# Optimization experiments

Hardware: AMD Instinct MI355X
Metric: run time of the kernel (lower is better)

Reference implementation:

```python
import jax, jax.numpy as jnp
import numpy as np

SCALING = 2.0  # alpha / r = 128 / 64


def setup_inputs() -> dict:
    key = jax.random.key(0)
    k1, k2, k3, k4 = jax.random.split(key, 4)
    in_f, out_f, r, tokens = 4096, 16384, 64, 64
    return {
        "x": jax.random.normal(k1, (tokens, in_f), dtype=jnp.float32),
        "weight": jax.random.normal(k2, (out_f, in_f), dtype=jnp.float32) * (1.0 / np.sqrt(in_f)),
        "lora_A": jax.random.normal(k3, (r, in_f), dtype=jnp.float32) * (1.0 / np.sqrt(in_f)),
        "lora_B": jax.random.normal(k4, (out_f, r), dtype=jnp.float32) * (1.0 / np.sqrt(r)),
    }


def reference(x, weight, lora_A, lora_B):
    # base GEMM: [T, in] @ [in, out] -> [T, out]
    base = x @ weight.T
    # low-rank adapter: ((x @ A^T) @ B^T) scaled
    lora = (x @ lora_A.T) @ lora_B.T
    return base + SCALING * lora
```

## Files before the change

kernel.cpp:

```cpp
#include <hip/hip_runtime.h>
#include <hip/hip_bf16.h>

typedef __attribute__((ext_vector_type(8))) short bf16x8;
typedef __attribute__((ext_vector_type(4))) short s16x4;
typedef __attribute__((ext_vector_type(4))) float f32x4;

__device__ __forceinline__ short f2b(float f) {
    __hip_bfloat16 h = __float2bfloat16(f);
    return __builtin_bit_cast(short, h);
}

#define NPH 16
#define KC  256

__global__ void prep_kernel(const float* __restrict__ x,
                            const float* __restrict__ A,
                            ushort* __restrict__ xb,
                            ushort* __restrict__ yb) {
    const int tid = threadIdx.x, bid = blockIdx.x;

    const int gid = bid * 256 + tid;
    if (gid < 65536) {
        float4 v = ((const float4*)x)[gid];
        ushort4 s;
        s.x = (ushort)f2b(v.x); s.y = (ushort)f2b(v.y);
        s.z = (ushort)f2b(v.z); s.w = (ushort)f2b(v.w);
        ((ushort4*)xb)[gid] = s;
    }

    const int wave = tid >> 6, lane = tid & 63;
    const int idx = bid * 4 + wave;
    const int t = idx >> 6, r = idx & 63;
    const float4* xr = (const float4*)(x + (size_t)t * 4096);
    const float4* ar = (const float4*)(A + (size_t)r * 4096);
    float s = 0.f;
    #pragma unroll
    for (int i = 0; i < 16; ++i) {
        float4 a = xr[i * 64 + lane];
        float4 b = ar[i * 64 + lane];
        s += a.x * b.x + a.y * b.y + a.z * b.z + a.w * b.w;
    }
    #pragma unroll
    for (int off = 32; off; off >>= 1) s += __shfl_xor(s, off, 64);
    if (lane == 0) yb[idx] = (ushort)f2b(2.0f * s);
}

__global__ void __launch_bounds__(512)
lora_gemm(const float* __restrict__ W,
          const float* __restrict__ Bm,
          const ushort* __restrict__ xb,
          const ushort* __restrict__ yb,
          float* __restrict__ out) {
    __shared__ ushort buf[2][64 * KC];

    const int tid  = threadIdx.x;
    const int w    = tid >> 6;
    const int lane = tid & 63;
    const int j0   = blockIdx.x << 6;

    if (w >= 4) {
        const int s = w - 4;
        f32x4 st[16];
        for (int p = 0; p < NPH; ++p) {
            char* dst = (char*)&buf[p & 1][0];
            #pragma unroll
            for (int i = 0; i < 16; ++i) {
                const float* src = W + (size_t)(j0 + s * 16 + i) * 4096
                                     + p * KC + lane * 4;
                st[i] = *(const f32x4*)src;
            }
            #pragma unroll
            for (int i = 0; i < 16; ++i) {
                const int q = s * 16 + i;
                s16x4 v;
                v[0] = f2b(st[i][0]); v[1] = f2b(st[i][1]);
                v[2] = f2b(st[i][2]); v[3] = f2b(st[i][3]);
                *(s16x4*)(dst + q * 512 + ((lane * 8) ^ ((q & 7) << 4))) = v;
            }
            asm volatile("s_waitcnt lgkmcnt(0)" ::: "memory");
            __builtin_amdgcn_s_barrier();
        }
        return;
    }

    const int c  = lane & 15;
    const int kg = lane >> 4;
    const ushort* xrow = xb + (size_t)(w * 16 + c) * 4096 + kg * 8;

    f32x4 acc[4];
    #pragma unroll
    for (int n = 0; n < 4; ++n) acc[n] = f32x4{0.f, 0.f, 0.f, 0.f};

    __builtin_amdgcn_s_barrier();

    for (int p = 0; p < NPH; ++p) {
        const char* lb = (const char*)&buf[p & 1][0];
        #pragma unroll
        for (int sl = 0; sl < 8; ++sl) {
            bf16x8 aa = *(const bf16x8*)(xrow + p * KC + sl * 32);
            #pragma unroll
            for (int n = 0; n < 4; ++n) {
                const int q = n * 16 + c;
                bf16x8 bb = *(const bf16x8*)(lb + q * 512
                    + ((sl * 64 + kg * 16) ^ ((q & 7) << 4)));
                acc[n] = __builtin_amdgcn_mfma_f32_16x16x32_bf16(
                    aa, bb, acc[n], 0, 0, 0);
            }
        }
        if (p + 1 < NPH) {
            asm volatile("s_waitcnt lgkmcnt(0)" ::: "memory");
            __builtin_amdgcn_s_barrier();
        }
    }

    {
        const ushort* y0 = yb + (size_t)(w * 16 + c) * 64 + kg * 8;
        #pragma unroll
        for (int n = 0; n < 4; ++n) {
            const float* br = Bm + (size_t)(j0 + n * 16 + c) * 64 + kg * 8;
            #pragma unroll
            for (int k = 0; k < 64; k += 32) {
                f32x4 w0 = *(const f32x4*)(br + k);
                f32x4 w1 = *(const f32x4*)(br + k + 4);
                bf16x8 bb;
                bb[0] = f2b(w0[0]); bb[1] = f2b(w0[1]);
                bb[2] = f2b(w0[2]); bb[3] = f2b(w0[3]);
                bb[4] = f2b(w1[0]); bb[5] = f2b(w1[1]);
                bb[6] = f2b(w1[2]); bb[7] = f2b(w1[3]);
                bf16x8 aa = *(const bf16x8*)(y0 + k);
                acc[n] = __builtin_amdgcn_mfma_f32_16x16x32_bf16(
                    aa, bb, acc[n], 0, 0, 0);
            }
        }
    }

    #pragma unroll
    for (int n = 0; n < 4; ++n) {
        float* op = out + j0 + n * 16 + c;
        #pragma unroll
        for (int r = 0; r < 4; ++r)
            op[(size_t)(w * 16 + kg * 4 + r) * 16384] = acc[n][r];
    }
}

extern "C" void kernel_launch(void* const* d_in, const int* in_sizes, int n_in,
                              void* d_out, int out_size, void* d_ws, size_t ws_size,
                              hipStream_t stream) {
    const float* x  = (const float*)d_in[0];
    const float* W  = (const float*)d_in[1];
    const float* A  = (const float*)d_in[2];
    const float* Bm = (const float*)d_in[3];
    float* out = (float*)d_out;

    ushort* xb = (ushort*)d_ws;
    ushort* yb = (ushort*)((char*)d_ws + 524288);

    prep_kernel<<<1024, 256, 0, stream>>>(x, A, xb, yb);
    lora_gemm<<<256, 512, 0, stream>>>(W, Bm, xb, yb, out);
}
```

Before: 64.99 us.

## Stream fp32 weight tiles directly to LDS with triple-buffered async loads

Producer waves now use global_load_lds to copy raw fp32 weight tiles straight into shared memory, with a three-stage buffer that keeps two phases in flight. The bf16 conversion moves from the producer side to the consumer waves after they read from LDS. The K chunk is halved so the fp32 tile fits the LDS budget. This removes the register round trip and the serial load-convert-store step on the producers, so the weight stream, the main memory cost, can overlap compute better. In exchange the consumers do more conversion work and read twice as many LDS bytes per tile.

Measured after the change: 64.91 us. About the same (-0.1%).

```diff
diff --git a/kernel.cpp b/kernel.cpp
--- a/kernel.cpp
+++ b/kernel.cpp
@@ -2,7 +2,6 @@
 #include <hip/hip_bf16.h>
 
 typedef __attribute__((ext_vector_type(8))) short bf16x8;
-typedef __attribute__((ext_vector_type(4))) short s16x4;
 typedef __attribute__((ext_vector_type(4))) float f32x4;
 
 __device__ __forceinline__ short f2b(float f) {
@@ -10,8 +9,8 @@
     return __builtin_bit_cast(short, h);
 }
 
-#define NPH 16
-#define KC  256
+#define NPH 32
+#define KC  128
 
 __global__ void prep_kernel(const float* __restrict__ x,
                             const float* __restrict__ A,
@@ -51,7 +50,7 @@
           const ushort* __restrict__ xb,
           const ushort* __restrict__ yb,
           float* __restrict__ out) {
-    __shared__ ushort buf[2][64 * KC];
+    __shared__ char buf[3][64 * 512];
 
     const int tid  = threadIdx.x;
     const int w    = tid >> 6;
@@ -60,26 +59,31 @@
 
     if (w >= 4) {
         const int s = w - 4;
-        f32x4 st[16];
-        for (int p = 0; p < NPH; ++p) {
-            char* dst = (char*)&buf[p & 1][0];
+        auto issue = [&](int p) {
+            char* dst = &buf[p % 3][0];
             #pragma unroll
-            for (int i = 0; i < 16; ++i) {
-                const float* src = W + (size_t)(j0 + s * 16 + i) * 4096
-                                     + p * KC + lane * 4;
-                st[i] = *(const f32x4*)src;
+            for (int i = 0; i < 8; ++i) {
+                const int qa = s * 16 + i * 2;
+                const int q  = qa + (lane >> 5);
+                const int b  = (lane & 31) * 16;
+                const char* src = (const char*)(W + (size_t)(j0 + q) * 4096
+                                                + (size_t)p * KC)
+                                  + (b ^ ((q & 7) << 4));
+                __builtin_amdgcn_global_load_lds(
+                    (const uint32_t*)src,
+                    (uint32_t*)(dst + qa * 512), 16, 0, 0);
             }
-            #pragma unroll
-            for (int i = 0; i < 16; ++i) {
-                const int q = s * 16 + i;
-                s16x4 v;
-                v[0] = f2b(st[i][0]); v[1] = f2b(st[i][1]);
-                v[2] = f2b(st[i][2]); v[3] = f2b(st[i][3]);
-                *(s16x4*)(dst + q * 512 + ((lane * 8) ^ ((q & 7) << 4))) = v;
-            }
-            asm volatile("s_waitcnt lgkmcnt(0)" ::: "memory");
+        };
+
+        issue(0);
+        issue(1);
+        for (int p = 0; p < NPH - 1; ++p) {
+            asm volatile("s_waitcnt vmcnt(8)" ::: "memory");
             __builtin_amdgcn_s_barrier();
+            if (p + 2 < NPH) issue(p + 2);
         }
+        asm volatile("s_waitcnt vmcnt(0)" ::: "memory");
+        __builtin_amdgcn_s_barrier();
         return;
     }
 
@@ -91,25 +95,27 @@
     #pragma unroll
     for (int n = 0; n < 4; ++n) acc[n] = f32x4{0.f, 0.f, 0.f, 0.f};
 
-    __builtin_amdgcn_s_barrier();
-
     for (int p = 0; p < NPH; ++p) {
-        const char* lb = (const char*)&buf[p & 1][0];
+        __builtin_amdgcn_s_barrier();
+        const char* lb = &buf[p % 3][0];
         #pragma unroll
-        for (int sl = 0; sl < 8; ++sl) {
+        for (int sl = 0; sl < 4; ++sl) {
             bf16x8 aa = *(const bf16x8*)(xrow + p * KC + sl * 32);
             #pragma unroll
             for (int n = 0; n < 4; ++n) {
-                const int q = n * 16 + c;
-                bf16x8 bb = *(const bf16x8*)(lb + q * 512
-                    + ((sl * 64 + kg * 16) ^ ((q & 7) << 4)));
+                const int q   = n * 16 + c;
+                const int swz = (q & 7) << 4;
+                const char* base = lb + q * 512;
+                f32x4 w0 = *(const f32x4*)(base + ((sl * 128 + kg * 32) ^ swz));
+                f32x4 w1 = *(const f32x4*)(base + ((sl * 128 + kg * 32 + 16) ^ swz));
+                bf16x8 bb;
+                bb[0] = f2b(w0[0]); bb[1] = f2b(w0[1]);
+                bb[2] = f2b(w0[2]); bb[3] = f2b(w0[3]);
+                bb[4] = f2b(w1[0]); bb[5] = f2b(w1[1]);
+                bb[6] = f2b(w1[2]); bb[7] = f2b(w1[3]);
                 acc[n] = __builtin_amdgcn_mfma_f32_16x16x32_bf16(
                     aa, bb, acc[n], 0, 0, 0);
             }
-        }
-        if (p + 1 < NPH) {
-            asm volatile("s_waitcnt lgkmcnt(0)" ::: "memory");
-            __builtin_amdgcn_s_barrier();
         }
     }
 
```

## Deepen producer pipeline for W with register prefetch and 4-slot LDS ring

Applied to the files above, without the earlier changes.

The producer waves now keep six K-chunks of W loads in flight in registers, using explicit vmcnt waits, and convert them into a 4-buffer LDS ring with half-size K chunks. The consumer waves synchronize once per chunk through a barrier schedule. Each block also starts at a rotated K offset so concurrent blocks read different column ranges of W and x. The aim is to hide HBM latency for the dominant streaming of W, in exchange for intricate hand-counted barriers and higher register pressure under launch_bounds(512,2).

After: 65.25 us. About the same (+0.4%).

```diff
diff --git a/kernel.cpp b/kernel.cpp
--- a/kernel.cpp
+++ b/kernel.cpp
@@ -10,8 +10,8 @@
     return __builtin_bit_cast(short, h);
 }
 
-#define NPH 16
-#define KC  256
+#define NPH 32
+#define KC  128
 
 __global__ void prep_kernel(const float* __restrict__ x,
                             const float* __restrict__ A,
@@ -45,41 +45,80 @@
     if (lane == 0) yb[idx] = (ushort)f2b(2.0f * s);
 }
 
-__global__ void __launch_bounds__(512)
+__global__ void __launch_bounds__(512, 2)
 lora_gemm(const float* __restrict__ W,
           const float* __restrict__ Bm,
           const ushort* __restrict__ xb,
           const ushort* __restrict__ yb,
           float* __restrict__ out) {
-    __shared__ ushort buf[2][64 * KC];
+    __shared__ char buf[4][64 * 256];
 
     const int tid  = threadIdx.x;
     const int w    = tid >> 6;
     const int lane = tid & 63;
     const int j0   = blockIdx.x << 6;
+    const int p0   = blockIdx.x & 31;
 
     if (w >= 4) {
-        const int s = w - 4;
-        f32x4 st[16];
-        for (int p = 0; p < NPH; ++p) {
-            char* dst = (char*)&buf[p & 1][0];
-            #pragma unroll
-            for (int i = 0; i < 16; ++i) {
-                const float* src = W + (size_t)(j0 + s * 16 + i) * 4096
-                                     + p * KC + lane * 4;
-                st[i] = *(const f32x4*)src;
-            }
-            #pragma unroll
-            for (int i = 0; i < 16; ++i) {
-                const int q = s * 16 + i;
-                s16x4 v;
-                v[0] = f2b(st[i][0]); v[1] = f2b(st[i][1]);
-                v[2] = f2b(st[i][2]); v[3] = f2b(st[i][3]);
-                *(s16x4*)(dst + q * 512 + ((lane * 8) ^ ((q & 7) << 4))) = v;
-            }
-            asm volatile("s_waitcnt lgkmcnt(0)" ::: "memory");
-            __builtin_amdgcn_s_barrier();
-        }
+        const int s16 = (w - 4) * 16;
+        f32x4 R0[8], R1[8], R2[8], R3[8], R4[8], R5[8];
+
+        #define ISSUE(BK, I)                                                \
+            if ((I) < NPH) {                                                \
+                const int p_ = (p0 + (I)) & 31;                             \
+                _Pragma("unroll")                                           \
+                for (int k = 0; k < 8; ++k) {                               \
+                    const int q_ = s16 + k * 2 + (lane >> 5);               \
+                    BK[k] = *(const f32x4*)((const char*)(W                 \
+                        + (size_t)(j0 + q_) * 4096 + (size_t)p_ * KC)       \
+                        + (lane & 31) * 16);                                \
+                } }
+
+        #define CVTW(BK, B)                                                 \
+            { char* dst_ = &buf[B][0];                                      \
+              _Pragma("unroll")                                             \
+              for (int k = 0; k < 8; ++k) {                                 \
+                  const int q_ = s16 + k * 2 + (lane >> 5);                 \
+                  s16x4 v_;                                                 \
+                  v_[0] = f2b(BK[k][0]); v_[1] = f2b(BK[k][1]);             \
+                  v_[2] = f2b(BK[k][2]); v_[3] = f2b(BK[k][3]);             \
+                  *(s16x4*)(dst_ + q_ * 256                                 \
+                      + (((lane & 31) * 8) ^ ((q_ & 7) << 4))) = v_;        \
+              } }
+
+        #define VM(N) asm volatile("s_waitcnt vmcnt(" #N ")" ::: "memory");
+        #define LG()  asm volatile("s_waitcnt lgkmcnt(0)" ::: "memory");
+        #define BAR() __builtin_amdgcn_s_barrier();
+
+        ISSUE(R0, 0) ISSUE(R1, 1) ISSUE(R2, 2)
+        ISSUE(R3, 3) ISSUE(R4, 4) ISSUE(R5, 5)
+        VM(40) CVTW(R0, 0) LG() ISSUE(R0, 6)
+        VM(40) CVTW(R1, 1) LG() ISSUE(R1, 7)
+        VM(40) CVTW(R2, 2) LG() ISSUE(R2, 8)
+        BAR()
+
+        #define STEP(BK, B, I9) VM(40) CVTW(BK, B) LG() ISSUE(BK, I9) BAR()
+        STEP(R3, 3,  9) STEP(R4, 0, 10) STEP(R5, 1, 11) STEP(R0, 2, 12)
+        STEP(R1, 3, 13) STEP(R2, 0, 14) STEP(R3, 1, 15) STEP(R4, 2, 16)
+        STEP(R5, 3, 17) STEP(R0, 0, 18) STEP(R1, 1, 19) STEP(R2, 2, 20)
+        STEP(R3, 3, 21) STEP(R4, 0, 22) STEP(R5, 1, 23) STEP(R0, 2, 24)
+        STEP(R1, 3, 25) STEP(R2, 0, 26) STEP(R3, 1, 27) STEP(R4, 2, 28)
+        STEP(R5, 3, 29) STEP(R0, 0, 30) STEP(R1, 1, 31)
+
+        VM(40) CVTW(R2, 2) LG() BAR()
+        VM(32) CVTW(R3, 3) LG() BAR()
+        VM(24) CVTW(R4, 0) LG() BAR()
+        VM(16) CVTW(R5, 1) LG() BAR()
+        VM(8)  CVTW(R0, 2) LG() BAR()
+        VM(0)  CVTW(R1, 3) LG() BAR()
+        BAR()
+        BAR()
+        #undef STEP
+        #undef ISSUE
+        #undef CVTW
+        #undef VM
+        #undef LG
+        #undef BAR
         return;
     }
 
@@ -91,25 +130,21 @@
     #pragma unroll
     for (int n = 0; n < 4; ++n) acc[n] = f32x4{0.f, 0.f, 0.f, 0.f};
 
-    __builtin_amdgcn_s_barrier();
-
-    for (int p = 0; p < NPH; ++p) {
-        const char* lb = (const char*)&buf[p & 1][0];
+    for (int i = 0; i < NPH; ++i) {
+        const int p = (p0 + i) & 31;
+        __builtin_amdgcn_s_barrier();
+        const char* lb = &buf[i & 3][0];
         #pragma unroll
-        for (int sl = 0; sl < 8; ++sl) {
+        for (int sl = 0; sl < 4; ++sl) {
             bf16x8 aa = *(const bf16x8*)(xrow + p * KC + sl * 32);
             #pragma unroll
             for (int n = 0; n < 4; ++n) {
                 const int q = n * 16 + c;
-                bf16x8 bb = *(const bf16x8*)(lb + q * 512
+                bf16x8 bb = *(const bf16x8*)(lb + q * 256
                     + ((sl * 64 + kg * 16) ^ ((q & 7) << 4)));
                 acc[n] = __builtin_amdgcn_mfma_f32_16x16x32_bf16(
                     aa, bb, acc[n], 0, 0, 0);
             }
-        }
-        if (p + 1 < NPH) {
-            asm volatile("s_waitcnt lgkmcnt(0)" ::: "memory");
-            __builtin_amdgcn_s_barrier();
         }
     }
 
```
